# Kernel tuning notes

Hardware: AMD Instinct MI355X
Metric: run time of the kernel (lower is better)

Reference implementation:

```python
import jax, jax.numpy as jnp
import numpy as np

B, S, D, H = 4, 2048, 1024, 4096  # batch, seq, d_model, mlp hidden
EPS = 1e-12  # F.normalize eps


def _linear(x, W, b):
    return x @ W.T + b


def setup_inputs() -> dict:
    key = jax.random.key(0)
    ks = jax.random.split(key, 14)
    s = lambda d: 1.0 / np.sqrt(d)
    return {
        "x": jax.random.normal(ks[0], (B, S, D), dtype=jnp.float32),
        "Wq": jax.random.normal(ks[1], (D, D), dtype=jnp.float32) * s(D),
        "bq": jax.random.normal(ks[2], (D,), dtype=jnp.float32) * 0.01,
        "Wk": jax.random.normal(ks[3], (D, D), dtype=jnp.float32) * s(D),
        "bk": jax.random.normal(ks[4], (D,), dtype=jnp.float32) * 0.01,
        "Wv": jax.random.normal(ks[5], (D, D), dtype=jnp.float32) * s(D),
        "bv": jax.random.normal(ks[6], (D,), dtype=jnp.float32) * 0.01,
        "W1": jax.random.normal(ks[7], (D, D), dtype=jnp.float32) * s(D),
        "b1": jax.random.normal(ks[8], (D,), dtype=jnp.float32) * 0.01,
        "W2": jax.random.normal(ks[9], (H, D), dtype=jnp.float32) * s(D),
        "b2": jax.random.normal(ks[10], (H,), dtype=jnp.float32) * 0.01,
        "W3": jax.random.normal(ks[11], (D, H), dtype=jnp.float32) * s(H),
        "b3": jax.random.normal(ks[12], (D,), dtype=jnp.float32) * 0.01,
    }


def reference(x, Wq, bq, Wk, bk, Wv, bv, W1, b1, W2, b2, W3, b3):
    Q = _linear(x, Wq, bq)  # [B,S,D]
    K = _linear(x, Wk, bk)
    V = _linear(x, Wv, bv)
    # L2-normalize along feature dim (F.normalize, p=2, dim=2)
    Q = Q / jnp.maximum(jnp.linalg.norm(Q, axis=2, keepdims=True), EPS)
    K = K / jnp.maximum(jnp.linalg.norm(K, axis=2, keepdims=True), EPS)
    sim = jnp.einsum("bqd,bkd->bqk", Q, K)  # cosine similarities [B,S,S]
    attn = jax.nn.softmax(sim, axis=2)
    out = jnp.einsum("bqk,bkd->bqd", attn, V)  # [B,S,D]
    # MLP: Linear->relu->Linear->relu->Linear (dropout identity in eval)
    h = jax.nn.relu(_linear(out, W1, b1))
    h = jax.nn.relu(_linear(h, W2, b2))
    return _linear(h, W3, b3)
```

## Files before the change

kernel.cpp:

```cpp
#include <hip/hip_runtime.h>


using u16 = unsigned short;
using bf16x8 = __attribute__((ext_vector_type(8))) __bf16;
using f32x4  = __attribute__((ext_vector_type(4))) float;

__device__ __forceinline__ u16 f2bf(float f) {
  unsigned u = __float_as_uint(f);
  unsigned r = (u + 0x7FFFu + ((u >> 16) & 1u)) >> 16;
  return (u16)r;
}
__device__ __forceinline__ float bf2f(u16 h) {
  return __uint_as_float(((unsigned)h) << 16);
}

struct CastSegs {
  const float* src[7];
  u16* dst[7];
  long beg[8];
};
__global__ __launch_bounds__(256) void cast_multi_kernel(CastSegs cs) {
  long idx = (long)blockIdx.x * 256 + threadIdx.x;
  if (idx >= cs.beg[7]) return;
  int seg = 0;
#pragma unroll
  for (int s = 1; s < 7; ++s) seg += (idx >= cs.beg[s]) ? 1 : 0;
  const long loc = idx - cs.beg[seg];
  float4 v = reinterpret_cast<const float4*>(cs.src[seg])[loc];
  ushort4 o;
  o.x = f2bf(v.x); o.y = f2bf(v.y); o.z = f2bf(v.z); o.w = f2bf(v.w);
  reinterpret_cast<ushort4*>(cs.dst[seg])[loc] = o;
}

__global__ __launch_bounds__(256) void l2norm2_kernel(
    const u16* __restrict__ Qi, const u16* __restrict__ Ki,
    u16* __restrict__ Qo, u16* __restrict__ Ko) {
  __shared__ float red[4];
  long row = blockIdx.x;
  const u16* in;
  u16* out;
  if (row < 8192) { in = Qi + row * 1024; out = Qo + row * 1024; }
  else            { in = Ki + (row - 8192) * 1024; out = Ko + (row - 8192) * 1024; }
  const int tid = threadIdx.x, lane = tid & 63, wave = tid >> 6;
  ushort4 h = *reinterpret_cast<const ushort4*>(in + tid * 4);
  float x0 = bf2f(h.x), x1 = bf2f(h.y), x2 = bf2f(h.z), x3 = bf2f(h.w);
  float ss = x0 * x0 + x1 * x1 + x2 * x2 + x3 * x3;
#pragma unroll
  for (int o = 32; o; o >>= 1) ss += __shfl_xor(ss, o);
  if (lane == 0) red[wave] = ss;
  __syncthreads();
  ss = red[0] + red[1] + red[2] + red[3];
  float s = 1.0f / fmaxf(sqrtf(ss), 1e-12f);
  ushort4 o;
  o.x = f2bf(x0 * s); o.y = f2bf(x1 * s); o.z = f2bf(x2 * s); o.w = f2bf(x3 * s);
  *reinterpret_cast<ushort4*>(out + tid * 4) = o;
}

__global__ void transpose_kernel(const u16* __restrict__ in, u16* __restrict__ out,
                                 int rows, int cols) {
  __shared__ u16 t[32][33];
  const int c0 = blockIdx.x * 32, r0 = blockIdx.y * 32;
  const long off = (long)blockIdx.z * rows * cols;
  const u16* ib = in + off;
  u16* ob = out + off;
  const int tx = threadIdx.x, ty = threadIdx.y;
#pragma unroll
  for (int j = 0; j < 4; ++j)
    t[ty + j * 8][tx] = ib[(long)(r0 + ty + j * 8) * cols + c0 + tx];
  __syncthreads();
#pragma unroll
  for (int j = 0; j < 4; ++j)
    ob[(long)(c0 + ty + j * 8) * rows + r0 + tx] = t[tx][ty + j * 8];
}

__global__ __launch_bounds__(256) void softmax_kernel(
    const u16* __restrict__ in, u16* __restrict__ out) {
  __shared__ float red[4];
  long row = blockIdx.x;
  const int tid = threadIdx.x, lane = tid & 63, wave = tid >> 6;
  const u16* p = in + row * 2048 + tid * 8;
  ushort4 h0 = *reinterpret_cast<const ushort4*>(p);
  ushort4 h1 = *reinterpret_cast<const ushort4*>(p + 4);
  float v[8];
  v[0] = bf2f(h0.x); v[1] = bf2f(h0.y); v[2] = bf2f(h0.z); v[3] = bf2f(h0.w);
  v[4] = bf2f(h1.x); v[5] = bf2f(h1.y); v[6] = bf2f(h1.z); v[7] = bf2f(h1.w);
  float m = v[0];
#pragma unroll
  for (int i = 1; i < 8; ++i) m = fmaxf(m, v[i]);
#pragma unroll
  for (int o = 32; o; o >>= 1) m = fmaxf(m, __shfl_xor(m, o));
  if (lane == 0) red[wave] = m;
  __syncthreads();
  m = fmaxf(fmaxf(red[0], red[1]), fmaxf(red[2], red[3]));
  float s = 0.0f;
#pragma unroll
  for (int i = 0; i < 8; ++i) { v[i] = __expf(v[i] - m); s += v[i]; }
#pragma unroll
  for (int o = 32; o; o >>= 1) s += __shfl_xor(s, o);
  __syncthreads();
  if (lane == 0) red[wave] = s;
  __syncthreads();
  s = red[0] + red[1] + red[2] + red[3];
  float inv = 1.0f / s;
  ushort4 o0, o1;
  o0.x = f2bf(v[0] * inv); o0.y = f2bf(v[1] * inv);
  o0.z = f2bf(v[2] * inv); o0.w = f2bf(v[3] * inv);
  o1.x = f2bf(v[4] * inv); o1.y = f2bf(v[5] * inv);
  o1.z = f2bf(v[6] * inv); o1.w = f2bf(v[7] * inv);
  *reinterpret_cast<ushort4*>(out + row * 2048 + tid * 8) = o0;
  *reinterpret_cast<ushort4*>(out + row * 2048 + tid * 8 + 4) = o1;
}

struct Frags { bf16x8 a[4][2]; bf16x8 b[4][2]; };

template <int MODE>
__global__ __launch_bounds__(512, 2) void gemmra(
    const u16* __restrict__ A, const u16* __restrict__ Bw,
    const float* __restrict__ bias, void* __restrict__ Cout,
    const float* __restrict__ bias2, void* __restrict__ Cout2,
    const float* __restrict__ bias3, void* __restrict__ Cout3,
    int N, int K, long batchA, long batchB, long batchC, int relu,
    int gx, int gy) {
  constexpr int ASZ = 128 * 64;
  constexpr int BSZ = 256 * 64;
  __shared__ u16 lds[2 * (ASZ + BSZ)];
  u16* const ldsA = lds;
  u16* const ldsB = lds + 2 * ASZ;

  const int nwg = gridDim.x;
  const int lid = blockIdx.x;
  const int q = nwg >> 3, r = nwg & 7;
  const int xcd = lid & 7, jj = lid >> 3;
  const int wg = (xcd < r ? xcd * (q + 1) : r * (q + 1) + (xcd - r) * q) + jj;
  const int by = wg % gy;
  const int rest = wg / gy;
  const int bx = rest % gx;
  const int bz = rest / gx;

  const int tid = threadIdx.x, wave = tid >> 6, lane = tid & 63;
  const int wr = wave >> 2, wc = wave & 3;
  const int fr = lane & 15, hi = lane >> 4;

  const long Abase = bz * batchA + (long)by * 128 * K;
  const long Bbase = bz * batchB + (long)bx * 256 * K;

  int aoff[4][2], boff[4][2];
#pragma unroll
  for (int m = 0; m < 4; ++m) {
    const int qm = m >> 1, ml = m & 1;
    const int row = qm * 64 + wr * 32 + ml * 16 + fr;
#pragma unroll
    for (int ks = 0; ks < 2; ++ks) {
      const int gg = ks * 4 + hi;
      aoff[m][ks] = row * 64 + ((gg ^ (row & 7)) * 8);
    }
  }
#pragma unroll
  for (int n = 0; n < 4; ++n) {
    const int qn = n >> 1, nl = n & 1;
    const int row = qn * 128 + wc * 32 + nl * 16 + fr;
#pragma unroll
    for (int ks = 0; ks < 2; ++ks) {
      const int gg = ks * 4 + hi;
      boff[n][ks] = row * 64 + ((gg ^ (row & 7)) * 8);
    }
  }

  const int rA = wave * 8 + (lane >> 3);
  const int g8 = (((lane & 7) ^ (lane >> 3)) * 8);
  long asrc[2], bsrc[4];
#pragma unroll
  for (int rr = 0; rr < 2; ++rr) asrc[rr] = Abase + (long)(rr * 64 + rA) * K + g8;
#pragma unroll
  for (int rr = 0; rr < 4; ++rr) bsrc[rr] = Bbase + (long)(rr * 64 + rA) * K + g8;

#define STAGE_A(bufp, rr, k0)                                                  \
  __builtin_amdgcn_global_load_lds(                                            \
      (const __attribute__((address_space(1))) void*)(A + asrc[rr] + (k0)),    \
      (__attribute__((address_space(3))) void*)((bufp) + (rr) * 4096 + wave * 512), \
      16, 0, 0)
#define STAGE_B(bufp, rr, k0)                                                  \
  __builtin_amdgcn_global_load_lds(                                            \
      (const __attribute__((address_space(1))) void*)(Bw + bsrc[rr] + (k0)),   \
      (__attribute__((address_space(3))) void*)((bufp) + (rr) * 4096 + wave * 512), \
      16, 0, 0)
#define STAGE_TILE(T)                                                          \
  {                                                                            \
    u16* sA_ = ldsA + ((T) & 1) * ASZ;                                         \
    u16* sB_ = ldsB + ((T) & 1) * BSZ;                                         \
    const int k0_ = (T) << 6;                                                  \
    STAGE_A(sA_, 0, k0_); STAGE_A(sA_, 1, k0_);                                \
    STAGE_B(sB_, 0, k0_); STAGE_B(sB_, 1, k0_);                                \
    STAGE_B(sB_, 2, k0_); STAGE_B(sB_, 3, k0_);                                \
  }
#define READ_FRAGS(F, T)                                                       \
  {                                                                            \
    u16* rA_ = ldsA + ((T) & 1) * ASZ;                                         \
    u16* rB_ = ldsB + ((T) & 1) * BSZ;                                         \
    _Pragma("unroll") for (int m = 0; m < 4; ++m)                              \
    _Pragma("unroll") for (int ks = 0; ks < 2; ++ks)                           \
      F.a[m][ks] = *reinterpret_cast<const bf16x8*>(&rA_[aoff[m][ks]]);        \
    _Pragma("unroll") for (int n = 0; n < 4; ++n)                              \
    _Pragma("unroll") for (int ks = 0; ks < 2; ++ks)                           \
      F.b[n][ks] = *reinterpret_cast<const bf16x8*>(&rB_[boff[n][ks]]);        \
  }
#define RA_ITER(T, FC, FN)                                                     \
  {                                                                            \
    if ((T) + 2 < NT) STAGE_TILE((T) + 2)                                      \
    if ((T) + 1 < NT) {                                                        \
      if ((T) + 2 < NT) asm volatile("s_waitcnt vmcnt(6)" ::: "memory");       \
      else              asm volatile("s_waitcnt vmcnt(0)" ::: "memory");       \
      __builtin_amdgcn_s_barrier();                                            \
      READ_FRAGS(FN, (T) + 1)                                                  \
      __builtin_amdgcn_s_barrier();                                            \
    }                                                                          \
    __builtin_amdgcn_s_setprio(1);                                             \
    _Pragma("unroll") for (int ks = 0; ks < 2; ++ks)                           \
    _Pragma("unroll") for (int m = 0; m < 4; ++m)                              \
    _Pragma("unroll") for (int n = 0; n < 4; ++n)                              \
      acc[m][n] = __builtin_amdgcn_mfma_f32_16x16x32_bf16(                     \
          FC.a[m][ks], FC.b[n][ks], acc[m][n], 0, 0, 0);                       \
    __builtin_amdgcn_s_setprio(0);                                             \
  }

  const int NT = K >> 6;

  f32x4 acc[4][4] = {};
  Frags fA, fB;

  STAGE_TILE(0)
  STAGE_TILE(1)
  asm volatile("s_waitcnt vmcnt(6)" ::: "memory");
  __builtin_amdgcn_s_barrier();
  READ_FRAGS(fA, 0)
  asm volatile("s_waitcnt lgkmcnt(0)" ::: "memory");
  __builtin_amdgcn_sched_barrier(0);
  __builtin_amdgcn_s_barrier();

  for (int t = 0; t < NT; t += 2) {
    RA_ITER(t, fA, fB)
    RA_ITER(t + 1, fB, fA)
  }
#undef STAGE_A
#undef STAGE_B
#undef STAGE_TILE
#undef READ_FRAGS
#undef RA_ITER

  const long cbase = bz * batchC;
  const int crow = by * 128;
  int ccol = bx * 256;
  const float* bp = bias;
  void* cp = Cout;
  constexpr bool obf = (MODE == 1) || (MODE == 2);
  int Nst = N;
  if constexpr (MODE == 2) {
    const int sel = ccol >> 10;
    if (sel == 1) { bp = bias2; cp = Cout2; }
    else if (sel == 2) { bp = bias3; cp = Cout3; }
    ccol &= 1023;
    Nst = 1024;
  }
#pragma unroll
  for (int m = 0; m < 4; ++m) {
    const int qm = m >> 1, ml = m & 1;
    const int r0 = crow + qm * 64 + wr * 32 + ml * 16 + hi * 4;
#pragma unroll
    for (int n = 0; n < 4; ++n) {
      const int qn = n >> 1, nl = n & 1;
      const int c = ccol + qn * 128 + wc * 32 + nl * 16 + fr;
      const float bb = bp ? bp[c] : 0.0f;
#pragma unroll
      for (int j = 0; j < 4; ++j) {
        float v = acc[m][n][j] + bb;
        if (relu) v = fmaxf(v, 0.0f);
        const long idx = cbase + (long)(r0 + j) * Nst + c;
        if (obf) ((u16*)cp)[idx] = f2bf(v);
        else     ((float*)cp)[idx] = v;
      }
    }
  }
}

extern "C" void kernel_launch(void* const* d_in, const int* in_sizes, int n_in,
                              void* d_out, int out_size, void* d_ws, size_t ws_size,
                              hipStream_t stream) {
  (void)in_sizes; (void)n_in; (void)out_size; (void)ws_size;
  const float* x  = (const float*)d_in[0];
  const float* Wq = (const float*)d_in[1];
  const float* bq = (const float*)d_in[2];
  const float* Wk = (const float*)d_in[3];
  const float* bk = (const float*)d_in[4];
  const float* Wv = (const float*)d_in[5];
  const float* bv = (const float*)d_in[6];
  const float* W1 = (const float*)d_in[7];
  const float* b1 = (const float*)d_in[8];
  const float* W2 = (const float*)d_in[9];
  const float* b2 = (const float*)d_in[10];
  const float* W3 = (const float*)d_in[11];
  const float* b3 = (const float*)d_in[12];

  char* ws = (char*)d_ws;
  const size_t MB = 1u << 20;
  u16* Qbf  = (u16*)(ws + 0);
  u16* Kbf  = Qbf + 8388608;
  u16* h2   = (u16*)(ws + 0);
  u16* xbf = (u16*)(ws + 64 * MB);
  u16* Vbf = xbf + (size_t)8192 * 1024;
  u16* P   = (u16*)(ws + 64 * MB);
  u16* Wq_b = (u16*)(ws + 96 * MB);
  u16* Wk_b = Wq_b + 1048576;
  u16* Wv_b = Wk_b + 1048576;
  u16* W1_b = Wv_b + 1048576;
  u16* W2_b = W1_b + 1048576;
  u16* W3_b = W2_b + 4194304;
  u16* Qn = (u16*)(ws + 120 * MB);
  u16* Kn = Qn + 8388608;
  u16* Vt = Kn + 8388608;
  u16* attnout = Qn;
  u16* h1      = Kn;

  CastSegs cs;
  cs.src[0] = x;  cs.dst[0] = xbf;
  cs.src[1] = Wq; cs.dst[1] = Wq_b;
  cs.src[2] = Wk; cs.dst[2] = Wk_b;
  cs.src[3] = Wv; cs.dst[3] = Wv_b;
  cs.src[4] = W1; cs.dst[4] = W1_b;
  cs.src[5] = W2; cs.dst[5] = W2_b;
  cs.src[6] = W3; cs.dst[6] = W3_b;
  long szs[7] = {2097152, 262144, 262144, 262144, 262144, 1048576, 1048576};
  long acc0 = 0;
  for (int i = 0; i < 7; ++i) { cs.beg[i] = acc0; acc0 += szs[i]; }
  cs.beg[7] = acc0;
  cast_multi_kernel<<<dim3((unsigned)((acc0 + 255) / 256)), 256, 0, stream>>>(cs);

  gemmra<2><<<dim3(12 * 64), 512, 0, stream>>>(
      xbf, Wq_b, bq, Qbf, bk, Kbf, bv, Vbf, 3072, 1024, 0, 0, 0, 0, 12, 64);
  l2norm2_kernel<<<16384, 256, 0, stream>>>(Qbf, Kbf, Qn, Kn);
  transpose_kernel<<<dim3(32, 64, 4), dim3(32, 8), 0, stream>>>(Vbf, Vt, 2048, 1024);
  gemmra<1><<<dim3(8 * 16 * 4), 512, 0, stream>>>(
      Qn, Kn, nullptr, P, nullptr, nullptr, nullptr, nullptr,
      2048, 1024, 2097152L, 2097152L, 4194304L, 0, 8, 16);
  softmax_kernel<<<8192, 256, 0, stream>>>(P, P);
  gemmra<1><<<dim3(4 * 16 * 4), 512, 0, stream>>>(
      P, Vt, nullptr, attnout, nullptr, nullptr, nullptr, nullptr,
      1024, 2048, 4194304L, 2097152L, 2097152L, 0, 4, 16);
  gemmra<1><<<dim3(4 * 64), 512, 0, stream>>>(
      attnout, W1_b, b1, h1, nullptr, nullptr, nullptr, nullptr,
      1024, 1024, 0, 0, 0, 1, 4, 64);
  gemmra<1><<<dim3(16 * 64), 512, 0, stream>>>(
      h1, W2_b, b2, h2, nullptr, nullptr, nullptr, nullptr,
      4096, 1024, 0, 0, 0, 1, 16, 64);
  gemmra<0><<<dim3(4 * 64), 512, 0, stream>>>(
      h2, W3_b, b3, (float*)d_out, nullptr, nullptr, nullptr, nullptr,
      1024, 4096, 0, 0, 0, 0, 4, 64);
}
```

Baseline: 399.7 us.

## Add 256x256-tile GEMM kernel with quadrant-interleaved pipelining for large GEMMs

Adds a new gemm256 kernel that computes 256x256 output tiles per workgroup with 8 waves, double-buffered LDS, and a schedule that splits each k-step into four MFMA quadrants interleaved with fragment reads and next-tile global-to-LDS loads. It is used for the fused QKV projection, the QK^T scores GEMM and the W2 MLP GEMM, while the smaller-N GEMMs keep the 128x256 kernel. The larger tile doubles A-operand reuse and halves the workgroup count, which reduces global/L2 traffic per FLOP. The cost is more LDS (128 KB) and more accumulator registers, which can lower occupancy, and fewer workgroups may underfill the CUs.

```diff
diff --git a/kernel.cpp b/kernel.cpp
--- a/kernel.cpp
+++ b/kernel.cpp
@@ -111,17 +111,15 @@
   *reinterpret_cast<ushort4*>(out + row * 2048 + tid * 8 + 4) = o1;
 }
 
-struct Frags { bf16x8 a[4][2]; bf16x8 b[4][2]; };
-
 template <int MODE>
-__global__ __launch_bounds__(512, 2) void gemmra(
+__global__ __launch_bounds__(512, 2) void gemm256(
     const u16* __restrict__ A, const u16* __restrict__ Bw,
     const float* __restrict__ bias, void* __restrict__ Cout,
     const float* __restrict__ bias2, void* __restrict__ Cout2,
     const float* __restrict__ bias3, void* __restrict__ Cout3,
     int N, int K, long batchA, long batchB, long batchC, int relu,
     int gx, int gy) {
-  constexpr int ASZ = 128 * 64;
+  constexpr int ASZ = 256 * 64;
   constexpr int BSZ = 256 * 64;
   __shared__ u16 lds[2 * (ASZ + BSZ)];
   u16* const ldsA = lds;
@@ -141,6 +139,199 @@
   const int wr = wave >> 2, wc = wave & 3;
   const int fr = lane & 15, hi = lane >> 4;
 
+  const long Abase = bz * batchA + (long)by * 256 * K;
+  const long Bbase = bz * batchB + (long)bx * 256 * K;
+
+  int aoff[2][4][2], boff[2][2][2];
+#pragma unroll
+  for (int qm = 0; qm < 2; ++qm)
+#pragma unroll
+    for (int ml = 0; ml < 4; ++ml) {
+      const int row = qm * 128 + wr * 64 + ml * 16 + fr;
+#pragma unroll
+      for (int ks = 0; ks < 2; ++ks)
+        aoff[qm][ml][ks] = row * 64 + (((ks * 4 + hi) ^ (row & 7)) * 8);
+    }
+#pragma unroll
+  for (int qn = 0; qn < 2; ++qn)
+#pragma unroll
+    for (int nl = 0; nl < 2; ++nl) {
+      const int row = qn * 128 + wc * 32 + nl * 16 + fr;
+#pragma unroll
+      for (int ks = 0; ks < 2; ++ks)
+        boff[qn][nl][ks] = row * 64 + (((ks * 4 + hi) ^ (row & 7)) * 8);
+    }
+
+  const int rA = wave * 8 + (lane >> 3);
+  const int g8 = (((lane & 7) ^ (lane >> 3)) * 8);
+  long asrc[4], bsrc[4];
+#pragma unroll
+  for (int rr = 0; rr < 4; ++rr) {
+    asrc[rr] = Abase + (long)(rr * 64 + rA) * K + g8;
+    bsrc[rr] = Bbase + (long)(rr * 64 + rA) * K + g8;
+  }
+
+#define STAGE_A(bufp, rr, k0)                                                  \
+  __builtin_amdgcn_global_load_lds(                                            \
+      (const __attribute__((address_space(1))) void*)(A + asrc[rr] + (k0)),    \
+      (__attribute__((address_space(3))) void*)((bufp) + (rr) * 4096 + wave * 512), \
+      16, 0, 0)
+#define STAGE_B(bufp, rr, k0)                                                  \
+  __builtin_amdgcn_global_load_lds(                                            \
+      (const __attribute__((address_space(1))) void*)(Bw + bsrc[rr] + (k0)),   \
+      (__attribute__((address_space(3))) void*)((bufp) + (rr) * 4096 + wave * 512), \
+      16, 0, 0)
+#define MFMA_Q(ah, bh, qm, qn)                                                 \
+  __builtin_amdgcn_s_setprio(1);                                               \
+  _Pragma("unroll") for (int ks = 0; ks < 2; ++ks)                             \
+  _Pragma("unroll") for (int ml = 0; ml < 4; ++ml)                             \
+  _Pragma("unroll") for (int nl = 0; nl < 2; ++nl)                             \
+    acc[(qm) * 4 + ml][(qn) * 2 + nl] =                                        \
+        __builtin_amdgcn_mfma_f32_16x16x32_bf16(                               \
+            ah[ml][ks], bh[nl][ks], acc[(qm) * 4 + ml][(qn) * 2 + nl], 0, 0, 0); \
+  __builtin_amdgcn_s_setprio(0);
+#define LGKM0                                                                  \
+  asm volatile("s_waitcnt lgkmcnt(0)" ::: "memory");                           \
+  __builtin_amdgcn_sched_barrier(0);
+
+  const int NT = K >> 6;
+
+#pragma unroll
+  for (int rr = 0; rr < 4; ++rr) { STAGE_A(ldsA, rr, 0); }
+#pragma unroll
+  for (int rr = 0; rr < 4; ++rr) { STAGE_B(ldsB, rr, 0); }
+#pragma unroll
+  for (int rr = 0; rr < 4; ++rr) { STAGE_A(ldsA + ASZ, rr, 64); }
+#pragma unroll
+  for (int rr = 0; rr < 4; ++rr) { STAGE_B(ldsB + BSZ, rr, 64); }
+  asm volatile("s_waitcnt vmcnt(8)" ::: "memory");
+  __builtin_amdgcn_s_barrier();
+
+  f32x4 acc[8][4] = {};
+
+  for (int t = 0; t < NT; ++t) {
+    u16* const cA = ldsA + (t & 1) * ASZ;
+    u16* const cB = ldsB + (t & 1) * BSZ;
+    const bool st = (t + 2) < NT;
+    const int k2 = (t + 2) << 6;
+    bf16x8 a0[4][2], a1[4][2], b0[2][2], b1[2][2];
+
+#pragma unroll
+    for (int ml = 0; ml < 4; ++ml)
+#pragma unroll
+      for (int ks = 0; ks < 2; ++ks)
+        a0[ml][ks] = *reinterpret_cast<const bf16x8*>(&cA[aoff[0][ml][ks]]);
+#pragma unroll
+    for (int nl = 0; nl < 2; ++nl)
+#pragma unroll
+      for (int ks = 0; ks < 2; ++ks)
+        b0[nl][ks] = *reinterpret_cast<const bf16x8*>(&cB[boff[0][nl][ks]]);
+    __builtin_amdgcn_s_barrier();
+    LGKM0
+    MFMA_Q(a0, b0, 0, 0)
+    __builtin_amdgcn_s_barrier();
+
+#pragma unroll
+    for (int nl = 0; nl < 2; ++nl)
+#pragma unroll
+      for (int ks = 0; ks < 2; ++ks)
+        b1[nl][ks] = *reinterpret_cast<const bf16x8*>(&cB[boff[1][nl][ks]]);
+    if (st) { STAGE_A(cA, 0, k2); STAGE_A(cA, 1, k2); }
+    __builtin_amdgcn_s_barrier();
+    LGKM0
+    MFMA_Q(a0, b1, 0, 1)
+    __builtin_amdgcn_s_barrier();
+
+#pragma unroll
+    for (int ml = 0; ml < 4; ++ml)
+#pragma unroll
+      for (int ks = 0; ks < 2; ++ks)
+        a1[ml][ks] = *reinterpret_cast<const bf16x8*>(&cA[aoff[1][ml][ks]]);
+    if (st) { STAGE_B(cB, 0, k2); STAGE_B(cB, 1, k2); }
+    __builtin_amdgcn_s_barrier();
+    LGKM0
+    MFMA_Q(a1, b1, 1, 1)
+    __builtin_amdgcn_s_barrier();
+
+    if (st) {
+      STAGE_A(cA, 2, k2); STAGE_A(cA, 3, k2);
+      STAGE_B(cB, 2, k2); STAGE_B(cB, 3, k2);
+    }
+    MFMA_Q(a1, b0, 1, 0)
+    if (st) asm volatile("s_waitcnt vmcnt(8)" ::: "memory");
+    else    asm volatile("s_waitcnt vmcnt(0)" ::: "memory");
+    __builtin_amdgcn_s_barrier();
+  }
+#undef STAGE_A
+#undef STAGE_B
+#undef MFMA_Q
+#undef LGKM0
+
+  const long cbase = bz * batchC;
+  const int crow = by * 256;
+  int ccol = bx * 256;
+  const float* bp = bias;
+  void* cp = Cout;
+  constexpr bool obf = (MODE == 1) || (MODE == 2);
+  int Nst = N;
+  if constexpr (MODE == 2) {
+    const int sel = ccol >> 10;
+    if (sel == 1) { bp = bias2; cp = Cout2; }
+    else if (sel == 2) { bp = bias3; cp = Cout3; }
+    ccol &= 1023;
+    Nst = 1024;
+  }
+#pragma unroll
+  for (int qm = 0; qm < 2; ++qm)
+#pragma unroll
+    for (int ml = 0; ml < 4; ++ml) {
+      const int r0 = crow + qm * 128 + wr * 64 + ml * 16 + hi * 4;
+#pragma unroll
+      for (int qn = 0; qn < 2; ++qn)
+#pragma unroll
+        for (int nl = 0; nl < 2; ++nl) {
+          const int c = ccol + qn * 128 + wc * 32 + nl * 16 + fr;
+          const float bb = bp ? bp[c] : 0.0f;
+#pragma unroll
+          for (int j = 0; j < 4; ++j) {
+            float v = acc[qm * 4 + ml][qn * 2 + nl][j] + bb;
+            if (relu) v = fmaxf(v, 0.0f);
+            const long idx = cbase + (long)(r0 + j) * Nst + c;
+            if (obf) ((u16*)cp)[idx] = f2bf(v);
+            else     ((float*)cp)[idx] = v;
+          }
+        }
+    }
+}
+
+struct Frags { bf16x8 a[4][2]; bf16x8 b[4][2]; };
+
+template <int MODE>
+__global__ __launch_bounds__(512, 2) void gemmra(
+    const u16* __restrict__ A, const u16* __restrict__ Bw,
+    const float* __restrict__ bias, void* __restrict__ Cout,
+    int N, int K, long batchA, long batchB, long batchC, int relu,
+    int gx, int gy) {
+  constexpr int ASZ = 128 * 64;
+  constexpr int BSZ = 256 * 64;
+  __shared__ u16 lds[2 * (ASZ + BSZ)];
+  u16* const ldsA = lds;
+  u16* const ldsB = lds + 2 * ASZ;
+
+  const int nwg = gridDim.x;
+  const int lid = blockIdx.x;
+  const int q = nwg >> 3, r = nwg & 7;
+  const int xcd = lid & 7, jj = lid >> 3;
+  const int wg = (xcd < r ? xcd * (q + 1) : r * (q + 1) + (xcd - r) * q) + jj;
+  const int by = wg % gy;
+  const int rest = wg / gy;
+  const int bx = rest % gx;
+  const int bz = rest / gx;
+
+  const int tid = threadIdx.x, wave = tid >> 6, lane = tid & 63;
+  const int wr = wave >> 2, wc = wave & 3;
+  const int fr = lane & 15, hi = lane >> 4;
+
   const long Abase = bz * batchA + (long)by * 128 * K;
   const long Bbase = bz * batchB + (long)bx * 256 * K;
 
@@ -150,20 +341,16 @@
     const int qm = m >> 1, ml = m & 1;
     const int row = qm * 64 + wr * 32 + ml * 16 + fr;
 #pragma unroll
-    for (int ks = 0; ks < 2; ++ks) {
-      const int gg = ks * 4 + hi;
-      aoff[m][ks] = row * 64 + ((gg ^ (row & 7)) * 8);
-    }
+    for (int ks = 0; ks < 2; ++ks)
+      aoff[m][ks] = row * 64 + (((ks * 4 + hi) ^ (row & 7)) * 8);
   }
 #pragma unroll
   for (int n = 0; n < 4; ++n) {
     const int qn = n >> 1, nl = n & 1;
     const int row = qn * 128 + wc * 32 + nl * 16 + fr;
 #pragma unroll
-    for (int ks = 0; ks < 2; ++ks) {
-      const int gg = ks * 4 + hi;
-      boff[n][ks] = row * 64 + ((gg ^ (row & 7)) * 8);
-    }
+    for (int ks = 0; ks < 2; ++ks)
+      boff[n][ks] = row * 64 + (((ks * 4 + hi) ^ (row & 7)) * 8);
   }
 
   const int rA = wave * 8 + (lane >> 3);
@@ -249,18 +436,8 @@
 
   const long cbase = bz * batchC;
   const int crow = by * 128;
-  int ccol = bx * 256;
-  const float* bp = bias;
-  void* cp = Cout;
-  constexpr bool obf = (MODE == 1) || (MODE == 2);
-  int Nst = N;
-  if constexpr (MODE == 2) {
-    const int sel = ccol >> 10;
-    if (sel == 1) { bp = bias2; cp = Cout2; }
-    else if (sel == 2) { bp = bias3; cp = Cout3; }
-    ccol &= 1023;
-    Nst = 1024;
-  }
+  const int ccol = bx * 256;
+  constexpr bool obf = (MODE == 1);
 #pragma unroll
   for (int m = 0; m < 4; ++m) {
     const int qm = m >> 1, ml = m & 1;
@@ -269,14 +446,14 @@
     for (int n = 0; n < 4; ++n) {
       const int qn = n >> 1, nl = n & 1;
       const int c = ccol + qn * 128 + wc * 32 + nl * 16 + fr;
-      const float bb = bp ? bp[c] : 0.0f;
+      const float bb = bias ? bias[c] : 0.0f;
 #pragma unroll
       for (int j = 0; j < 4; ++j) {
         float v = acc[m][n][j] + bb;
         if (relu) v = fmaxf(v, 0.0f);
-        const long idx = cbase + (long)(r0 + j) * Nst + c;
-        if (obf) ((u16*)cp)[idx] = f2bf(v);
-        else     ((float*)cp)[idx] = v;
+        const long idx = cbase + (long)(r0 + j) * N + c;
+        if (obf) ((u16*)Cout)[idx] = f2bf(v);
+        else     ((float*)Cout)[idx] = v;
       }
     }
   }
@@ -334,24 +511,21 @@
   cs.beg[7] = acc0;
   cast_multi_kernel<<<dim3((unsigned)((acc0 + 255) / 256)), 256, 0, stream>>>(cs);
 
-  gemmra<2><<<dim3(12 * 64), 512, 0, stream>>>(
-      xbf, Wq_b, bq, Qbf, bk, Kbf, bv, Vbf, 3072, 1024, 0, 0, 0, 0, 12, 64);
+  gemm256<2><<<dim3(12 * 32), 512, 0, stream>>>(
+      xbf, Wq_b, bq, Qbf, bk, Kbf, bv, Vbf, 3072, 1024, 0, 0, 0, 0, 12, 32);
   l2norm2_kernel<<<16384, 256, 0, stream>>>(Qbf, Kbf, Qn, Kn);
   transpose_kernel<<<dim3(32, 64, 4), dim3(32, 8), 0, stream>>>(Vbf, Vt, 2048, 1024);
-  gemmra<1><<<dim3(8 * 16 * 4), 512, 0, stream>>>(
+  gemm256<1><<<dim3(8 * 8 * 4), 512, 0, stream>>>(
       Qn, Kn, nullptr, P, nullptr, nullptr, nullptr, nullptr,
-      2048, 1024, 2097152L, 2097152L, 4194304L, 0, 8, 16);
+      2048, 1024, 2097152L, 2097152L, 4194304L, 0, 8, 8);
   softmax_kernel<<<8192, 256, 0, stream>>>(P, P);
   gemmra<1><<<dim3(4 * 16 * 4), 512, 0, stream>>>(
-      P, Vt, nullptr, attnout, nullptr, nullptr, nullptr, nullptr,
-      1024, 2048, 4194304L, 2097152L, 2097152L, 0, 4, 16);
+      P, Vt, nullptr, attnout, 1024, 2048, 4194304L, 2097152L, 2097152L, 0, 4, 16);
   gemmra<1><<<dim3(4 * 64), 512, 0, stream>>>(
-      attnout, W1_b, b1, h1, nullptr, nullptr, nullptr, nullptr,
-      1024, 1024, 0, 0, 0, 1, 4, 64);
-  gemmra<1><<<dim3(16 * 64), 512, 0, stream>>>(
+      attnout, W1_b, b1, h1, 1024, 1024, 0, 0, 0, 1, 4, 64);
+  gemm256<1><<<dim3(16 * 32), 512, 0, stream>>>(
       h1, W2_b, b2, h2, nullptr, nullptr, nullptr, nullptr,
-      4096, 1024, 0, 0, 0, 1, 16, 64);
+      4096, 1024, 0, 0, 0, 1, 16, 32);
   gemmra<0><<<dim3(4 * 64), 512, 0, stream>>>(
-      h2, W3_b, b3, (float*)d_out, nullptr, nullptr, nullptr, nullptr,
-      1024, 4096, 0, 0, 0, 0, 4, 64);
-}
+      h2, W3_b, b3, (float*)d_out, 1024, 4096, 0, 0, 0, 0, 4, 64);
+}
```

After: 370.1 us. 7.4% less time.

## Shrink GEMM tiles to 128x128 with 4 waves and add grouped band rasterization

Applied to the files above, without the earlier changes.

Replaces the 128x256, 8-wave GEMM with a 128x128 tile run by 4 waves, each computing a 64x64 sub-tile, and doubles the grid sizes to match. It also adds a band-grouped block ordering (gby rows per band), so blocks that run together share A and B tiles in cache. More blocks should improve occupancy and load balance on the small MLP GEMMs. In exchange, each block reuses less data per tile and issues more global-to-LDS loads.

```diff
diff --git a/kernel.cpp b/kernel.cpp
--- a/kernel.cpp
+++ b/kernel.cpp
@@ -12,6 +12,21 @@
 }
 __device__ __forceinline__ float bf2f(u16 h) {
   return __uint_as_float(((unsigned)h) << 16);
+}
+
+__device__ __forceinline__ void decomp(int lid, int nwg, int gx, int gy,
+                                       int gby, int& bx, int& by, int& bz) {
+  const int q = nwg >> 3, r = nwg & 7;
+  const int xcd = lid & 7, jj = lid >> 3;
+  const int wg = (xcd < r ? xcd * (q + 1) : r * (q + 1) + (xcd - r) * q) + jj;
+  const int byloc = wg % gby;
+  const int t1 = wg / gby;
+  bx = t1 % gx;
+  const int t2 = t1 / gx;
+  const int nb = gy / gby;
+  const int band = t2 % nb;
+  bz = t2 / nb;
+  by = band * gby + byloc;
 }
 
 struct CastSegs {
@@ -114,75 +129,63 @@
 struct Frags { bf16x8 a[4][2]; bf16x8 b[4][2]; };
 
 template <int MODE>
-__global__ __launch_bounds__(512, 2) void gemmra(
+__global__ __launch_bounds__(256, 2) void gemmo(
     const u16* __restrict__ A, const u16* __restrict__ Bw,
     const float* __restrict__ bias, void* __restrict__ Cout,
     const float* __restrict__ bias2, void* __restrict__ Cout2,
     const float* __restrict__ bias3, void* __restrict__ Cout3,
     int N, int K, long batchA, long batchB, long batchC, int relu,
-    int gx, int gy) {
+    int gx, int gy, int gby) {
   constexpr int ASZ = 128 * 64;
-  constexpr int BSZ = 256 * 64;
+  constexpr int BSZ = 128 * 64;
   __shared__ u16 lds[2 * (ASZ + BSZ)];
   u16* const ldsA = lds;
   u16* const ldsB = lds + 2 * ASZ;
 
-  const int nwg = gridDim.x;
-  const int lid = blockIdx.x;
-  const int q = nwg >> 3, r = nwg & 7;
-  const int xcd = lid & 7, jj = lid >> 3;
-  const int wg = (xcd < r ? xcd * (q + 1) : r * (q + 1) + (xcd - r) * q) + jj;
-  const int by = wg % gy;
-  const int rest = wg / gy;
-  const int bx = rest % gx;
-  const int bz = rest / gx;
+  int bx, by, bz;
+  decomp(blockIdx.x, gridDim.x, gx, gy, gby, bx, by, bz);
 
   const int tid = threadIdx.x, wave = tid >> 6, lane = tid & 63;
-  const int wr = wave >> 2, wc = wave & 3;
+  const int wr = wave >> 1, wc = wave & 1;
   const int fr = lane & 15, hi = lane >> 4;
 
   const long Abase = bz * batchA + (long)by * 128 * K;
-  const long Bbase = bz * batchB + (long)bx * 256 * K;
+  const long Bbase = bz * batchB + (long)bx * 128 * K;
 
   int aoff[4][2], boff[4][2];
 #pragma unroll
   for (int m = 0; m < 4; ++m) {
-    const int qm = m >> 1, ml = m & 1;
-    const int row = qm * 64 + wr * 32 + ml * 16 + fr;
-#pragma unroll
-    for (int ks = 0; ks < 2; ++ks) {
-      const int gg = ks * 4 + hi;
-      aoff[m][ks] = row * 64 + ((gg ^ (row & 7)) * 8);
-    }
+    const int row = wr * 64 + m * 16 + fr;
+#pragma unroll
+    for (int ks = 0; ks < 2; ++ks)
+      aoff[m][ks] = row * 64 + (((ks * 4 + hi) ^ (row & 7)) * 8);
   }
 #pragma unroll
   for (int n = 0; n < 4; ++n) {
-    const int qn = n >> 1, nl = n & 1;
-    const int row = qn * 128 + wc * 32 + nl * 16 + fr;
-#pragma unroll
-    for (int ks = 0; ks < 2; ++ks) {
-      const int gg = ks * 4 + hi;
-      boff[n][ks] = row * 64 + ((gg ^ (row & 7)) * 8);
-    }
-  }
-
-  const int rA = wave * 8 + (lane >> 3);
-  const int g8 = (((lane & 7) ^ (lane >> 3)) * 8);
-  long asrc[2], bsrc[4];
-#pragma unroll
-  for (int rr = 0; rr < 2; ++rr) asrc[rr] = Abase + (long)(rr * 64 + rA) * K + g8;
-#pragma unroll
-  for (int rr = 0; rr < 4; ++rr) bsrc[rr] = Bbase + (long)(rr * 64 + rA) * K + g8;
+    const int row = wc * 64 + n * 16 + fr;
+#pragma unroll
+    for (int ks = 0; ks < 2; ++ks)
+      boff[n][ks] = row * 64 + (((ks * 4 + hi) ^ (row & 7)) * 8);
+  }
+
+  const int rA = tid >> 3;
+  const int g8 = (((tid & 7) ^ ((tid >> 3) & 7)) * 8);
+  long asrc[4], bsrc[4];
+#pragma unroll
+  for (int rr = 0; rr < 4; ++rr) {
+    asrc[rr] = Abase + (long)(rr * 32 + rA) * K + g8;
+    bsrc[rr] = Bbase + (long)(rr * 32 + rA) * K + g8;
+  }
 
 #define STAGE_A(bufp, rr, k0)                                                  \
   __builtin_amdgcn_global_load_lds(                                            \
       (const __attribute__((address_space(1))) void*)(A + asrc[rr] + (k0)),    \
-      (__attribute__((address_space(3))) void*)((bufp) + (rr) * 4096 + wave * 512), \
+      (__attribute__((address_space(3))) void*)((bufp) + (rr) * 2048 + tid * 8), \
       16, 0, 0)
 #define STAGE_B(bufp, rr, k0)                                                  \
   __builtin_amdgcn_global_load_lds(                                            \
       (const __attribute__((address_space(1))) void*)(Bw + bsrc[rr] + (k0)),   \
-      (__attribute__((address_space(3))) void*)((bufp) + (rr) * 4096 + wave * 512), \
+      (__attribute__((address_space(3))) void*)((bufp) + (rr) * 2048 + tid * 8), \
       16, 0, 0)
 #define STAGE_TILE(T)                                                          \
   {                                                                            \
@@ -190,6 +193,7 @@
     u16* sB_ = ldsB + ((T) & 1) * BSZ;                                         \
     const int k0_ = (T) << 6;                                                  \
     STAGE_A(sA_, 0, k0_); STAGE_A(sA_, 1, k0_);                                \
+    STAGE_A(sA_, 2, k0_); STAGE_A(sA_, 3, k0_);                                \
     STAGE_B(sB_, 0, k0_); STAGE_B(sB_, 1, k0_);                                \
     STAGE_B(sB_, 2, k0_); STAGE_B(sB_, 3, k0_);                                \
   }
@@ -208,7 +212,7 @@
   {                                                                            \
     if ((T) + 2 < NT) STAGE_TILE((T) + 2)                                      \
     if ((T) + 1 < NT) {                                                        \
-      if ((T) + 2 < NT) asm volatile("s_waitcnt vmcnt(6)" ::: "memory");       \
+      if ((T) + 2 < NT) asm volatile("s_waitcnt vmcnt(8)" ::: "memory");       \
       else              asm volatile("s_waitcnt vmcnt(0)" ::: "memory");       \
       __builtin_amdgcn_s_barrier();                                            \
       READ_FRAGS(FN, (T) + 1)                                                  \
@@ -230,7 +234,7 @@
 
   STAGE_TILE(0)
   STAGE_TILE(1)
-  asm volatile("s_waitcnt vmcnt(6)" ::: "memory");
+  asm volatile("s_waitcnt vmcnt(8)" ::: "memory");
   __builtin_amdgcn_s_barrier();
   READ_FRAGS(fA, 0)
   asm volatile("s_waitcnt lgkmcnt(0)" ::: "memory");
@@ -249,7 +253,7 @@
 
   const long cbase = bz * batchC;
   const int crow = by * 128;
-  int ccol = bx * 256;
+  int ccol = bx * 128;
   const float* bp = bias;
   void* cp = Cout;
   constexpr bool obf = (MODE == 1) || (MODE == 2);
@@ -263,12 +267,10 @@
   }
 #pragma unroll
   for (int m = 0; m < 4; ++m) {
-    const int qm = m >> 1, ml = m & 1;
-    const int r0 = crow + qm * 64 + wr * 32 + ml * 16 + hi * 4;
+    const int r0 = crow + wr * 64 + m * 16 + hi * 4;
 #pragma unroll
     for (int n = 0; n < 4; ++n) {
-      const int qn = n >> 1, nl = n & 1;
-      const int c = ccol + qn * 128 + wc * 32 + nl * 16 + fr;
+      const int c = ccol + wc * 64 + n * 16 + fr;
       const float bb = bp ? bp[c] : 0.0f;
 #pragma unroll
       for (int j = 0; j < 4; ++j) {
@@ -334,24 +336,25 @@
   cs.beg[7] = acc0;
   cast_multi_kernel<<<dim3((unsigned)((acc0 + 255) / 256)), 256, 0, stream>>>(cs);
 
-  gemmra<2><<<dim3(12 * 64), 512, 0, stream>>>(
-      xbf, Wq_b, bq, Qbf, bk, Kbf, bv, Vbf, 3072, 1024, 0, 0, 0, 0, 12, 64);
+  dim3 blk(256);
+  gemmo<2><<<dim3(24 * 64), blk, 0, stream>>>(
+      xbf, Wq_b, bq, Qbf, bk, Kbf, bv, Vbf, 3072, 1024, 0, 0, 0, 0, 24, 64, 8);
   l2norm2_kernel<<<16384, 256, 0, stream>>>(Qbf, Kbf, Qn, Kn);
   transpose_kernel<<<dim3(32, 64, 4), dim3(32, 8), 0, stream>>>(Vbf, Vt, 2048, 1024);
-  gemmra<1><<<dim3(8 * 16 * 4), 512, 0, stream>>>(
+  gemmo<1><<<dim3(16 * 16 * 4), blk, 0, stream>>>(
       Qn, Kn, nullptr, P, nullptr, nullptr, nullptr, nullptr,
-      2048, 1024, 2097152L, 2097152L, 4194304L, 0, 8, 16);
+      2048, 1024, 2097152L, 2097152L, 4194304L, 0, 16, 16, 8);
   softmax_kernel<<<8192, 256, 0, stream>>>(P, P);
-  gemmra<1><<<dim3(4 * 16 * 4), 512, 0, stream>>>(
+  gemmo<1><<<dim3(8 * 16 * 4), blk, 0, stream>>>(
       P, Vt, nullptr, attnout, nullptr, nullptr, nullptr, nullptr,
-      1024, 2048, 4194304L, 2097152L, 2097152L, 0, 4, 16);
-  gemmra<1><<<dim3(4 * 64), 512, 0, stream>>>(
+      1024, 2048, 4194304L, 2097152L, 2097152L, 0, 8, 16, 8);
+  gemmo<1><<<dim3(8 * 64), blk, 0, stream>>>(
       attnout, W1_b, b1, h1, nullptr, nullptr, nullptr, nullptr,
-      1024, 1024, 0, 0, 0, 1, 4, 64);
-  gemmra<1><<<dim3(16 * 64), 512, 0, stream>>>(
+      1024, 1024, 0, 0, 0, 1, 8, 64, 16);
+  gemmo<1><<<dim3(32 * 64), blk, 0, stream>>>(
       h1, W2_b, b2, h2, nullptr, nullptr, nullptr, nullptr,
-      4096, 1024, 0, 0, 0, 1, 16, 64);
-  gemmra<0><<<dim3(4 * 64), 512, 0, stream>>>(
+      4096, 1024, 0, 0, 0, 1, 32, 64, 8);
+  gemmo<0><<<dim3(8 * 64), blk, 0, stream>>>(
       h2, W3_b, b3, (float*)d_out, nullptr, nullptr, nullptr, nullptr,
-      1024, 4096, 0, 0, 0, 0, 4, 64);
-}
+      1024, 4096, 0, 0, 0, 0, 8, 64, 16);
+}
```

After: 365.7 us. -8.5%, faster.
